# Kernel optimization log

Measured on AMD Instinct MI355X. Metric: run time of the kernel, lower is better.

## Reference

```python
import jax, jax.numpy as jnp
import numpy as np


def setup_inputs() -> dict:
    key = jax.random.key(0)
    k1, k2, k3, k4 = jax.random.split(key, 4)
    N, F_in, F_out = 8192, 512, 256
    inp = jax.random.normal(k1, (N, F_in), dtype=jnp.float32)
    adj = jax.random.uniform(k2, (N, N), dtype=jnp.float32)
    stdv = 1.0 / np.sqrt(F_out)
    weight = jax.random.uniform(k3, (F_in, F_out), minval=-stdv, maxval=stdv, dtype=jnp.float32)
    b = jax.random.uniform(k4, (F_out,), minval=-stdv, maxval=stdv, dtype=jnp.float32)
    return {"input": inp, "adj": adj, "weight": weight, "b": b}


def reference(input, adj, weight, b):
    N = adj.shape[0]
    degree = jnp.sum(adj, axis=1)                      # [N]
    # A_tilde = 2*I - adj
    A_tilde = 2.0 * jnp.eye(N, dtype=adj.dtype) - adj
    d_inv_sqrt = 1.0 / jnp.sqrt(2.0 + degree)          # [N]
    # D^-1/2 @ A_tilde @ D^-1/2 as broadcasted row/col scaling (same math, O(N^2))
    L_sharpen = d_inv_sqrt[:, None] * A_tilde * d_inv_sqrt[None, :]
    support = input @ weight                           # [N, F_out]
    out = L_sharpen @ support + b                      # [N, F_out]
    return jax.nn.relu(out)
```

## Files before the change

kernel.cpp:

```cpp
#include <hip/hip_runtime.h>


typedef _Float16 h4 __attribute__((ext_vector_type(4)));
typedef _Float16 h8 __attribute__((ext_vector_type(8)));
typedef float f4 __attribute__((ext_vector_type(4)));

__device__ __forceinline__ void gload_lds16(const void* g, void* l) {
    __builtin_amdgcn_global_load_lds(
        (const __attribute__((address_space(1))) void*)g,
        (__attribute__((address_space(3))) void*)l, 16, 0, 0);
}
__device__ __forceinline__ void gload2(const float* p, f4& x, f4& y) {
    asm volatile("global_load_dwordx4 %0, %2, off\n\t"
                 "global_load_dwordx4 %1, %2, off offset:16"
                 : "=&v"(x), "=&v"(y) : "v"(p) : "memory");
}
__device__ __forceinline__ void gloadBfrag(const char* p, h8& x, h8& y) {
    asm volatile("global_load_dwordx4 %0, %2, off\n\t"
                 "global_load_dwordx4 %1, %2, off offset:1024"
                 : "=&v"(x), "=&v"(y) : "v"(p) : "memory");
}

__global__ __launch_bounds__(256) void k0_wt(const float* __restrict__ weight,
                                             char* __restrict__ wt) {
    const int idx = blockIdx.x * 256 + threadIdx.x;
    const int k = idx >> 8, j = idx & 255;
    const _Float16 h = (_Float16)weight[idx];
    const int off = j * 1024 + ((k >> 6) << 7) + (((k & 63) << 1) ^ ((j & 7) << 4));
    *(_Float16*)(wt + off) = h;
}

__global__ __launch_bounds__(512) void k12_fused(const float* __restrict__ input,
                                                 const float* __restrict__ adj,
                                                 const char* __restrict__ wt,
                                                 float* __restrict__ dinv,
                                                 char* __restrict__ sT) {
    __shared__ char smem[4096 + 32768];
    const int bid = (int)blockIdx.x, t = (int)threadIdx.x;

    if (bid >= 256) {
        const int r = bid - 256;
        const float4* rp = (const float4*)(adj + (size_t)r * 8192);
        float s = 0.f;
#pragma unroll
        for (int i = 0; i < 4; ++i) {
            float4 v = rp[t + i * 512];
            s += (v.x + v.y) + (v.z + v.w);
        }
#pragma unroll
        for (int off = 32; off > 0; off >>= 1) s += __shfl_down(s, off, 64);
        float* part = (float*)smem;
        if ((t & 63) == 0) part[t >> 6] = s;
        __syncthreads();
        if (t == 0) {
            float deg = ((part[0] + part[1]) + (part[2] + part[3])) +
                        ((part[4] + part[5]) + (part[6] + part[7]));
            dinv[r] = 1.0f / sqrtf(2.0f + deg);
        }
        return;
    }

    const int w = t >> 6, l = t & 63;
    const int r0 = bid * 32;
    const int arow = t >> 4, ak4 = t & 15;
    const int bj = l >> 3, bb = (l & 7) * 16;

    f4 acc[2][2] = {};

    for (int kt = 0; kt < 8; ++kt) {
        const int k0 = kt * 64;
        __syncthreads();
        {
            float4 v = *(const float4*)(input + (size_t)(r0 + arow) * 512 + k0 + ak4 * 4);
            h4 h;
            h[0] = (_Float16)v.x; h[1] = (_Float16)v.y;
            h[2] = (_Float16)v.z; h[3] = (_Float16)v.w;
            *(h4*)(smem + arow * 128 + ((ak4 * 8) ^ ((arow & 7) << 4))) = h;
        }
#pragma unroll
        for (int q = 0; q < 4; ++q) {
            const int c = q * 8 + w;
            gload_lds16(wt + (size_t)(c * 8 + bj) * 1024 + kt * 128 + bb,
                        smem + 4096 + c * 1024);
        }
        __syncthreads();
#pragma unroll
        for (int kk = 0; kk < 2; ++kk) {
            const int ko = kk * 64 + ((l >> 4) << 4);
            h8 a[2], b[2];
#pragma unroll
            for (int m = 0; m < 2; ++m) {
                const int r = m * 16 + (l & 15);
                a[m] = *(const h8*)(smem + r * 128 + (ko ^ ((r & 7) << 4)));
            }
#pragma unroll
            for (int n = 0; n < 2; ++n) {
                const int j = w * 32 + n * 16 + (l & 15);
                b[n] = *(const h8*)(smem + 4096 + j * 128 + (ko ^ ((j & 7) << 4)));
            }
#pragma unroll
            for (int m = 0; m < 2; ++m)
#pragma unroll
                for (int n = 0; n < 2; ++n)
                    acc[m][n] = __builtin_amdgcn_mfma_f32_16x16x32_f16(a[m], b[n], acc[m][n], 0, 0, 0);
        }
    }
#pragma unroll
    for (int m = 0; m < 2; ++m)
#pragma unroll
        for (int n = 0; n < 2; ++n) {
            const int j = w * 32 + n * 16 + (l & 15);
            const int k0r = r0 + m * 16 + ((l >> 4) << 2);
            h4 h;
#pragma unroll
            for (int r = 0; r < 4; ++r)
                h[r] = (_Float16)acc[m][n][r];
            const int off = (((j >> 4) * 128 + (k0r >> 6)) << 11) +
                            (((k0r >> 5) & 1) << 10) +
                            ((((k0r >> 3) & 3) << 4) + (j & 15)) * 16 +
                            ((k0r & 7) << 1);
            *(h4*)(sT + off) = h;
        }
}

__global__ __launch_bounds__(512, 4) void k3_spmm(const float* __restrict__ adj,
                                                  const char* __restrict__ sT,
                                                  const float* __restrict__ dinvg,
                                                  _Float16* __restrict__ parth,
                                                  float* __restrict__ out,
                                                  int steps) {
    __shared__ __align__(16) char smem[2][8192];
    __shared__ __align__(16) float sdinv[2048];
    const int t = threadIdx.x;
    const int w = t >> 6, l = t & 63;
    const int i0 = (int)blockIdx.x * 64;
    const int ks0 = (int)blockIdx.y * steps * 64;
    const int dkt = (i0 - ks0) >> 6;

    const int arow = t >> 3;
    const int ak8 = (t & 7) * 8;
    const int arow_g = i0 + arow;
    const float* aptr = adj + (size_t)arow_g * 8192 + ks0 + ak8;
    const int a_off = arow * 128 + (((t & 7) << 4) ^ ((arow & 7) << 4));

    const char* bpn0 = sT + ((size_t)(w * 2) * 128 + (ks0 >> 6)) * 2048 + l * 16;
    const char* bpn1 = bpn0 + 262144;

    f4 acc[4][2] = {};
    h8 bvA[2][2], bvB[2][2];
    f4 ax0, ay0, ax1, ay1;

    auto loadB = [&](int kt, h8 (&bv)[2][2]) {
        gloadBfrag(bpn0 + (size_t)kt * 2048, bv[0][0], bv[1][0]);
        gloadBfrag(bpn1 + (size_t)kt * 2048, bv[0][1], bv[1][1]);
    };
    auto writeA = [&](char* buf, int kt, const f4 x, const f4 y) {
        const int kb = kt * 64 + ak8;
        const float4 d0 = *(const float4*)&sdinv[kb];
        const float4 d1 = *(const float4*)&sdinv[kb + 4];
        const int kg = ks0 + kb;
        h8 h;
        if (kt == dkt) {
            h[0] = (_Float16)(d0.x * ((arow_g == kg    ) ? 2.0f - x[0] : -x[0]));
            h[1] = (_Float16)(d0.y * ((arow_g == kg + 1) ? 2.0f - x[1] : -x[1]));
            h[2] = (_Float16)(d0.z * ((arow_g == kg + 2) ? 2.0f - x[2] : -x[2]));
            h[3] = (_Float16)(d0.w * ((arow_g == kg + 3) ? 2.0f - x[3] : -x[3]));
            h[4] = (_Float16)(d1.x * ((arow_g == kg + 4) ? 2.0f - y[0] : -y[0]));
            h[5] = (_Float16)(d1.y * ((arow_g == kg + 5) ? 2.0f - y[1] : -y[1]));
            h[6] = (_Float16)(d1.z * ((arow_g == kg + 6) ? 2.0f - y[2] : -y[2]));
            h[7] = (_Float16)(d1.w * ((arow_g == kg + 7) ? 2.0f - y[3] : -y[3]));
        } else {
            h[0] = (_Float16)(-d0.x * x[0]);
            h[1] = (_Float16)(-d0.y * x[1]);
            h[2] = (_Float16)(-d0.z * x[2]);
            h[3] = (_Float16)(-d0.w * x[3]);
            h[4] = (_Float16)(-d1.x * y[0]);
            h[5] = (_Float16)(-d1.y * y[1]);
            h[6] = (_Float16)(-d1.z * y[2]);
            h[7] = (_Float16)(-d1.w * y[3]);
        }
        *(h8*)(buf + a_off) = h;
    };
    auto compute = [&](const char* A, const h8 (&bv)[2][2]) {
        __builtin_amdgcn_s_setprio(1);
#pragma unroll
        for (int kk = 0; kk < 2; ++kk) {
            const int ko = kk * 64 + ((l >> 4) << 4);
            h8 a[4];
#pragma unroll
            for (int m = 0; m < 4; ++m) {
                const int r = m * 16 + (l & 15);
                a[m] = *(const h8*)(A + r * 128 + (ko ^ ((r & 7) << 4)));
            }
#pragma unroll
            for (int m = 0; m < 4; ++m)
#pragma unroll
                for (int n = 0; n < 2; ++n)
                    acc[m][n] = __builtin_amdgcn_mfma_f32_16x16x32_f16(a[m], bv[kk][n], acc[m][n], 0, 0, 0);
        }
        __builtin_amdgcn_s_setprio(0);
    };

#define SBAR0() __builtin_amdgcn_sched_barrier(0)
#define WAIT_ADJ(N, X, Y)                                                     \
    asm volatile("s_waitcnt vmcnt(" #N ")" : "+v"(X), "+v"(Y) :: "memory");   \
    SBAR0();
#define WAIT_STEP(N, X, Y, BV)                                                \
    asm volatile("s_waitcnt vmcnt(" #N ")"                                    \
                 : "+v"(X), "+v"(Y), "+v"(BV[0][0]), "+v"(BV[0][1]),          \
                   "+v"(BV[1][0]), "+v"(BV[1][1]) :: "memory");               \
    SBAR0();
#define WAIT_BV(N, BV)                                                        \
    asm volatile("s_waitcnt vmcnt(" #N ")"                                    \
                 : "+v"(BV[0][0]), "+v"(BV[0][1]),                            \
                   "+v"(BV[1][0]), "+v"(BV[1][1]) :: "memory");               \
    SBAR0();
#define BARRIER()                                                             \
    asm volatile("s_waitcnt lgkmcnt(0)\n\ts_barrier" ::: "memory");           \
    SBAR0();

    gload_lds16(dinvg + ks0 + t * 4, (char*)sdinv + w * 1024);
    gload2(aptr, ax0, ay0);
    loadB(0, bvA);
    WAIT_ADJ(4, ax0, ay0)
    asm volatile("s_barrier" ::: "memory");
    SBAR0();
    writeA(smem[0], 0, ax0, ay0);
    gload2(aptr + 64, ax1, ay1);
    BARRIER()

#define BODY(kt, XC, YC, XN, YN, BVC, BVN, BUFC, BUFN)                        \
    {                                                                         \
        loadB((kt) + 1, BVN);                                                 \
        gload2(aptr + (size_t)((kt) + 2) * 64, XC, YC);                       \
        WAIT_STEP(6, XN, YN, BVC)                                             \
        writeA(BUFN, (kt) + 1, XN, YN);                                       \
        compute(BUFC, BVC);                                                   \
        BARRIER()                                                             \
    }

    for (int kt2 = 0; kt2 + 2 <= steps - 2; kt2 += 2) {
        BODY(kt2,     ax0, ay0, ax1, ay1, bvA, bvB, smem[0], smem[1])
        BODY(kt2 + 1, ax1, ay1, ax0, ay0, bvB, bvA, smem[1], smem[0])
    }
    {
        loadB(steps - 1, bvB);
        WAIT_STEP(4, ax1, ay1, bvA)
        writeA(smem[1], steps - 1, ax1, ay1);
        compute(smem[0], bvA);
        BARRIER()
    }
    {
        WAIT_BV(0, bvB)
        compute(smem[1], bvB);
    }
#undef BODY
#undef WAIT_ADJ
#undef WAIT_STEP
#undef WAIT_BV
#undef BARRIER
#undef SBAR0

    if (blockIdx.y == gridDim.y - 1) {
#pragma unroll
        for (int m = 0; m < 4; ++m)
#pragma unroll
            for (int n = 0; n < 2; ++n) {
                const int j = w * 32 + n * 16 + (l & 15);
                const int ib = i0 + m * 16 + ((l >> 4) << 2);
#pragma unroll
                for (int r = 0; r < 4; ++r)
                    out[(size_t)(ib + r) * 256 + j] = acc[m][n][r];
            }
    } else {
        _Float16* pslot = parth + (size_t)blockIdx.y * (8192 * 256);
#pragma unroll
        for (int m = 0; m < 4; ++m)
#pragma unroll
            for (int n = 0; n < 2; ++n) {
                const int j = w * 32 + n * 16 + (l & 15);
                const int ib = i0 + m * 16 + ((l >> 4) << 2);
#pragma unroll
                for (int r = 0; r < 4; ++r)
                    pslot[(size_t)(ib + r) * 256 + j] = (_Float16)acc[m][n][r];
            }
    }
}

__global__ __launch_bounds__(256) void k4_fin(const _Float16* __restrict__ parth,
                                              float* __restrict__ out,
                                              const float* __restrict__ dinv,
                                              const float* __restrict__ bias,
                                              int nsplit) {
    const int idx = blockIdx.x * 256 + threadIdx.x;
    float4 s = ((const float4*)out)[idx];
    for (int sp = 0; sp < nsplit - 1; ++sp) {
        const h4 p = *(const h4*)(parth + (size_t)sp * (8192 * 256) + (size_t)idx * 4);
        s.x += (float)p[0]; s.y += (float)p[1];
        s.z += (float)p[2]; s.w += (float)p[3];
    }
    const float dv = dinv[idx >> 6];
    const float4 b = ((const float4*)bias)[idx & 63];
    float4 r;
    r.x = fmaxf(dv * s.x + b.x, 0.f);
    r.y = fmaxf(dv * s.y + b.y, 0.f);
    r.z = fmaxf(dv * s.z + b.z, 0.f);
    r.w = fmaxf(dv * s.w + b.w, 0.f);
    ((float4*)out)[idx] = r;
}

extern "C" void kernel_launch(void* const* d_in, const int* in_sizes, int n_in,
                              void* d_out, int out_size, void* d_ws, size_t ws_size,
                              hipStream_t stream) {
    const float* input  = (const float*)d_in[0];
    const float* adj    = (const float*)d_in[1];
    const float* weight = (const float*)d_in[2];
    const float* bias   = (const float*)d_in[3];
    float* out = (float*)d_out;

    char* ws = (char*)d_ws;
    float*    dinv  = (float*)ws;
    char*     wt    = ws + 32768;
    char*     sT    = ws + 294912;
    _Float16* parth = (_Float16*)(ws + 294912 + 4194304);

    const size_t base = 294912 + 4194304;
    int nsplit = 1;
    if (ws_size >= base + 3ull * 4194304) nsplit = 4;
    else if (ws_size >= base + 1ull * 4194304) nsplit = 2;
    const int steps = 128 / nsplit;

    k0_wt<<<512, 256, 0, stream>>>(weight, wt);
    k12_fused<<<8448, 512, 0, stream>>>(input, adj, wt, dinv, sT);
    k3_spmm<<<dim3(128, nsplit), 512, 0, stream>>>(adj, sT, dinv, parth, out, steps);
    k4_fin<<<2048, 256, 0, stream>>>(parth, out, dinv, bias, nsplit);
}
```

Measured before the change: 120.5 us.

## Halve k3 row tile, stage B fragments through LDS, raise occupancy

The SpMM kernel's row tile drops from 64 to 32 rows per block, which doubles the grid along the row dimension and raises launch bounds to 8 blocks per CU. B fragments are no longer held in registers; each wave copies its own B slice into LDS with global_load_lds right before computing on it. dinv values are now fetched from global memory alongside each adjacency chunk instead of being preloaded into shared memory. The aim is to cut register and LDS pressure so more waves stay resident and hide latency. In exchange, each B tile is reused across half as many rows, so L2 traffic for B doubles, and the B loads are no longer prefetched a step ahead, so their latency sits on the critical path.

```diff
diff --git a/kernel.cpp b/kernel.cpp
--- a/kernel.cpp
+++ b/kernel.cpp
@@ -10,15 +10,9 @@
         (const __attribute__((address_space(1))) void*)g,
         (__attribute__((address_space(3))) void*)l, 16, 0, 0);
 }
-__device__ __forceinline__ void gload2(const float* p, f4& x, f4& y) {
-    asm volatile("global_load_dwordx4 %0, %2, off\n\t"
-                 "global_load_dwordx4 %1, %2, off offset:16"
-                 : "=&v"(x), "=&v"(y) : "v"(p) : "memory");
-}
-__device__ __forceinline__ void gloadBfrag(const char* p, h8& x, h8& y) {
-    asm volatile("global_load_dwordx4 %0, %2, off\n\t"
-                 "global_load_dwordx4 %1, %2, off offset:1024"
-                 : "=&v"(x), "=&v"(y) : "v"(p) : "memory");
+__device__ __forceinline__ void gloadA1(const float* p, f4& x) {
+    asm volatile("global_load_dwordx4 %0, %1, off"
+                 : "=&v"(x) : "v"(p) : "memory");
 }
 
 __global__ __launch_bounds__(256) void k0_wt(const float* __restrict__ weight,
@@ -123,147 +117,135 @@
         }
 }
 
-__global__ __launch_bounds__(512, 4) void k3_spmm(const float* __restrict__ adj,
+__global__ __launch_bounds__(512, 8) void k3_spmm(const float* __restrict__ adj,
                                                   const char* __restrict__ sT,
                                                   const float* __restrict__ dinvg,
                                                   _Float16* __restrict__ parth,
                                                   float* __restrict__ out,
                                                   int steps) {
-    __shared__ __align__(16) char smem[2][8192];
-    __shared__ __align__(16) float sdinv[2048];
+    __shared__ __align__(16) char smemA[2][4096];
+    __shared__ __align__(16) char smemB[8][4096];
     const int t = threadIdx.x;
     const int w = t >> 6, l = t & 63;
-    const int i0 = (int)blockIdx.x * 64;
+    const int i0 = (int)blockIdx.x * 32;
     const int ks0 = (int)blockIdx.y * steps * 64;
     const int dkt = (i0 - ks0) >> 6;
 
-    const int arow = t >> 3;
-    const int ak8 = (t & 7) * 8;
+    const int arow = t >> 4;
+    const int ak4 = t & 15;
     const int arow_g = i0 + arow;
-    const float* aptr = adj + (size_t)arow_g * 8192 + ks0 + ak8;
-    const int a_off = arow * 128 + (((t & 7) << 4) ^ ((arow & 7) << 4));
-
-    const char* bpn0 = sT + ((size_t)(w * 2) * 128 + (ks0 >> 6)) * 2048 + l * 16;
-    const char* bpn1 = bpn0 + 262144;
-
-    f4 acc[4][2] = {};
-    h8 bvA[2][2], bvB[2][2];
-    f4 ax0, ay0, ax1, ay1;
-
-    auto loadB = [&](int kt, h8 (&bv)[2][2]) {
-        gloadBfrag(bpn0 + (size_t)kt * 2048, bv[0][0], bv[1][0]);
-        gloadBfrag(bpn1 + (size_t)kt * 2048, bv[0][1], bv[1][1]);
+    const float* aptr = adj + (size_t)arow_g * 8192 + ks0 + ak4 * 4;
+    const float* dptr = dinvg + ks0 + ak4 * 4;
+    const int a_off = arow * 128 + ((ak4 * 8) ^ ((arow & 7) << 4));
+
+    const char* bsrc = sT + ((size_t)(w * 2) * 128 + (ks0 >> 6)) * 2048 + l * 16;
+    char* bl = smemB[w];
+
+    f4 acc[2][2] = {};
+    f4 ax0, ax1, d0, d1;
+
+    auto stageB = [&](int kt) {
+        const char* s0 = bsrc + (size_t)kt * 2048;
+        gload_lds16(s0, bl);
+        gload_lds16(s0 + 1024, bl + 1024);
+        gload_lds16(s0 + 262144, bl + 2048);
+        gload_lds16(s0 + 262144 + 1024, bl + 3072);
     };
-    auto writeA = [&](char* buf, int kt, const f4 x, const f4 y) {
-        const int kb = kt * 64 + ak8;
-        const float4 d0 = *(const float4*)&sdinv[kb];
-        const float4 d1 = *(const float4*)&sdinv[kb + 4];
-        const int kg = ks0 + kb;
-        h8 h;
+    auto writeA = [&](char* buf, int kt, const f4 x, const f4 d) {
+        const int kg = ks0 + kt * 64 + ak4 * 4;
+        h4 h;
         if (kt == dkt) {
-            h[0] = (_Float16)(d0.x * ((arow_g == kg    ) ? 2.0f - x[0] : -x[0]));
-            h[1] = (_Float16)(d0.y * ((arow_g == kg + 1) ? 2.0f - x[1] : -x[1]));
-            h[2] = (_Float16)(d0.z * ((arow_g == kg + 2) ? 2.0f - x[2] : -x[2]));
-            h[3] = (_Float16)(d0.w * ((arow_g == kg + 3) ? 2.0f - x[3] : -x[3]));
-            h[4] = (_Float16)(d1.x * ((arow_g == kg + 4) ? 2.0f - y[0] : -y[0]));
-            h[5] = (_Float16)(d1.y * ((arow_g == kg + 5) ? 2.0f - y[1] : -y[1]));
-            h[6] = (_Float16)(d1.z * ((arow_g == kg + 6) ? 2.0f - y[2] : -y[2]));
-            h[7] = (_Float16)(d1.w * ((arow_g == kg + 7) ? 2.0f - y[3] : -y[3]));
+            h[0] = (_Float16)(d[0] * ((arow_g == kg    ) ? 2.0f - x[0] : -x[0]));
+            h[1] = (_Float16)(d[1] * ((arow_g == kg + 1) ? 2.0f - x[1] : -x[1]));
+            h[2] = (_Float16)(d[2] * ((arow_g == kg + 2) ? 2.0f - x[2] : -x[2]));
+            h[3] = (_Float16)(d[3] * ((arow_g == kg + 3) ? 2.0f - x[3] : -x[3]));
         } else {
-            h[0] = (_Float16)(-d0.x * x[0]);
-            h[1] = (_Float16)(-d0.y * x[1]);
-            h[2] = (_Float16)(-d0.z * x[2]);
-            h[3] = (_Float16)(-d0.w * x[3]);
-            h[4] = (_Float16)(-d1.x * y[0]);
-            h[5] = (_Float16)(-d1.y * y[1]);
-            h[6] = (_Float16)(-d1.z * y[2]);
-            h[7] = (_Float16)(-d1.w * y[3]);
-        }
-        *(h8*)(buf + a_off) = h;
+            h[0] = (_Float16)(-d[0] * x[0]);
+            h[1] = (_Float16)(-d[1] * x[1]);
+            h[2] = (_Float16)(-d[2] * x[2]);
+            h[3] = (_Float16)(-d[3] * x[3]);
+        }
+        *(h4*)(buf + a_off) = h;
     };
-    auto compute = [&](const char* A, const h8 (&bv)[2][2]) {
+    auto compute = [&](const char* A) {
         __builtin_amdgcn_s_setprio(1);
 #pragma unroll
         for (int kk = 0; kk < 2; ++kk) {
             const int ko = kk * 64 + ((l >> 4) << 4);
-            h8 a[4];
-#pragma unroll
-            for (int m = 0; m < 4; ++m) {
+            h8 a[2], b[2];
+#pragma unroll
+            for (int m = 0; m < 2; ++m) {
                 const int r = m * 16 + (l & 15);
                 a[m] = *(const h8*)(A + r * 128 + (ko ^ ((r & 7) << 4)));
             }
 #pragma unroll
-            for (int m = 0; m < 4; ++m)
+            for (int n = 0; n < 2; ++n)
+                b[n] = *(const h8*)(bl + n * 2048 + kk * 1024 + l * 16);
+#pragma unroll
+            for (int m = 0; m < 2; ++m)
 #pragma unroll
                 for (int n = 0; n < 2; ++n)
-                    acc[m][n] = __builtin_amdgcn_mfma_f32_16x16x32_f16(a[m], bv[kk][n], acc[m][n], 0, 0, 0);
+                    acc[m][n] = __builtin_amdgcn_mfma_f32_16x16x32_f16(a[m], b[n], acc[m][n], 0, 0, 0);
         }
         __builtin_amdgcn_s_setprio(0);
     };
 
 #define SBAR0() __builtin_amdgcn_sched_barrier(0)
-#define WAIT_ADJ(N, X, Y)                                                     \
-    asm volatile("s_waitcnt vmcnt(" #N ")" : "+v"(X), "+v"(Y) :: "memory");   \
+#define WAIT_VM0(X0, X1)                                                      \
+    asm volatile("s_waitcnt vmcnt(0)" : "+v"(X0), "+v"(X1) :: "memory");      \
     SBAR0();
-#define WAIT_STEP(N, X, Y, BV)                                                \
-    asm volatile("s_waitcnt vmcnt(" #N ")"                                    \
-                 : "+v"(X), "+v"(Y), "+v"(BV[0][0]), "+v"(BV[0][1]),          \
-                   "+v"(BV[1][0]), "+v"(BV[1][1]) :: "memory");               \
-    SBAR0();
-#define WAIT_BV(N, BV)                                                        \
-    asm volatile("s_waitcnt vmcnt(" #N ")"                                    \
-                 : "+v"(BV[0][0]), "+v"(BV[0][1]),                            \
-                   "+v"(BV[1][0]), "+v"(BV[1][1]) :: "memory");               \
+#define WAIT_STEP(X, D)                                                       \
+    asm volatile("s_waitcnt vmcnt(2)" : "+v"(X), "+v"(D) :: "memory");        \
     SBAR0();
 #define BARRIER()                                                             \
     asm volatile("s_waitcnt lgkmcnt(0)\n\ts_barrier" ::: "memory");           \
     SBAR0();
 
-    gload_lds16(dinvg + ks0 + t * 4, (char*)sdinv + w * 1024);
-    gload2(aptr, ax0, ay0);
-    loadB(0, bvA);
-    WAIT_ADJ(4, ax0, ay0)
-    asm volatile("s_barrier" ::: "memory");
-    SBAR0();
-    writeA(smem[0], 0, ax0, ay0);
-    gload2(aptr + 64, ax1, ay1);
+    gloadA1(dptr, d0);
+    gloadA1(aptr, ax0);
+    WAIT_VM0(ax0, d0)
+    writeA(smemA[0], 0, ax0, d0);
+    gloadA1(dptr + 64, d1);
+    gloadA1(aptr + 64, ax1);
     BARRIER()
 
-#define BODY(kt, XC, YC, XN, YN, BVC, BVN, BUFC, BUFN)                        \
+#define BODY(kt, AXC, DC, AXN, DN, BUFC, BUFN)                                \
     {                                                                         \
-        loadB((kt) + 1, BVN);                                                 \
-        gload2(aptr + (size_t)((kt) + 2) * 64, XC, YC);                       \
-        WAIT_STEP(6, XN, YN, BVC)                                             \
-        writeA(BUFN, (kt) + 1, XN, YN);                                       \
-        compute(BUFC, BVC);                                                   \
+        stageB(kt);                                                           \
+        gloadA1(dptr + (size_t)((kt) + 2) * 64, DC);                          \
+        gloadA1(aptr + (size_t)((kt) + 2) * 64, AXC);                         \
+        WAIT_STEP(AXN, DN)                                                    \
+        writeA(BUFN, (kt) + 1, AXN, DN);                                      \
+        compute(BUFC);                                                        \
         BARRIER()                                                             \
     }
 
     for (int kt2 = 0; kt2 + 2 <= steps - 2; kt2 += 2) {
-        BODY(kt2,     ax0, ay0, ax1, ay1, bvA, bvB, smem[0], smem[1])
-        BODY(kt2 + 1, ax1, ay1, ax0, ay0, bvB, bvA, smem[1], smem[0])
+        BODY(kt2,     ax0, d0, ax1, d1, smemA[0], smemA[1])
+        BODY(kt2 + 1, ax1, d1, ax0, d0, smemA[1], smemA[0])
     }
     {
-        loadB(steps - 1, bvB);
-        WAIT_STEP(4, ax1, ay1, bvA)
-        writeA(smem[1], steps - 1, ax1, ay1);
-        compute(smem[0], bvA);
+        stageB(steps - 2);
+        WAIT_VM0(ax1, d1)
+        writeA(smemA[1], steps - 1, ax1, d1);
+        compute(smemA[0]);
         BARRIER()
     }
     {
-        WAIT_BV(0, bvB)
-        compute(smem[1], bvB);
+        stageB(steps - 1);
+        asm volatile("s_waitcnt vmcnt(0)" ::: "memory");
+        SBAR0();
+        compute(smemA[1]);
     }
 #undef BODY
-#undef WAIT_ADJ
+#undef WAIT_VM0
 #undef WAIT_STEP
-#undef WAIT_BV
 #undef BARRIER
 #undef SBAR0
 
     if (blockIdx.y == gridDim.y - 1) {
 #pragma unroll
-        for (int m = 0; m < 4; ++m)
+        for (int m = 0; m < 2; ++m)
 #pragma unroll
             for (int n = 0; n < 2; ++n) {
                 const int j = w * 32 + n * 16 + (l & 15);
@@ -275,7 +257,7 @@
     } else {
         _Float16* pslot = parth + (size_t)blockIdx.y * (8192 * 256);
 #pragma unroll
-        for (int m = 0; m < 4; ++m)
+        for (int m = 0; m < 2; ++m)
 #pragma unroll
             for (int n = 0; n < 2; ++n) {
                 const int j = w * 32 + n * 16 + (l & 15);
@@ -332,6 +314,6 @@
 
     k0_wt<<<512, 256, 0, stream>>>(weight, wt);
     k12_fused<<<8448, 512, 0, stream>>>(input, adj, wt, dinv, sT);
-    k3_spmm<<<dim3(128, nsplit), 512, 0, stream>>>(adj, sT, dinv, parth, out, steps);
+    k3_spmm<<<dim3(256, nsplit), 512, 0, stream>>>(adj, sT, dinv, parth, out, steps);
     k4_fin<<<2048, 256, 0, stream>>>(parth, out, dinv, bias, nsplit);
 }
```

Result: slower. 145.4 us (+20.7%).
